# Optimization experiments

Measured on AMD Instinct MI355X. Metric: run time of the kernel, lower is better.

## Reference

```python
import jax, jax.numpy as jnp
import numpy as np

BLOCK = 128  # block_size=(128,128) from MoeFP8Matmul
E, H, I = 8, 2048, 2816  # experts, hidden, intermediate
T, K = 512, 2  # tokens, top-k

_FP8 = getattr(jnp, "float8_e4m3fn", jnp.float32)

def _dequant(w, s):
    # w: [N, Kd] fp8 values (stored fp32), s: [N//128, Kd//128] inverse scales
    s_full = jnp.repeat(jnp.repeat(s, BLOCK, axis=-2), BLOCK, axis=-1)
    return w * s_full

def setup_inputs() -> dict:
    key = jax.random.key(0)
    ks = jax.random.split(key, 7)
    x = jax.random.normal(ks[0], (T, H), dtype=jnp.float32)
    topk_ids = jax.random.randint(ks[1], (T, K), 0, E, dtype=jnp.int64)
    topk_weights = jax.random.uniform(ks[2], (T, K), dtype=jnp.float32)
    # fp8-representable weight values (round-trip through e4m3)
    w13 = (jax.random.normal(ks[3], (E, 2 * I, H), dtype=jnp.float32) * 0.5)
    w13_fp8 = w13.astype(_FP8).astype(jnp.float32)
    w2 = (jax.random.normal(ks[4], (E, H, I), dtype=jnp.float32) * 0.5)
    w2_fp8 = w2.astype(_FP8).astype(jnp.float32)
    w13_scale = jax.random.uniform(ks[5], (E, (2 * I) // BLOCK, H // BLOCK),
                                   dtype=jnp.float32, minval=0.5, maxval=1.5)
    w2_scale = jax.random.uniform(ks[6], (E, H // BLOCK, I // BLOCK),
                                  dtype=jnp.float32, minval=0.5, maxval=1.5)
    return {"x": x, "topk_ids": topk_ids, "topk_weights": topk_weights,
            "w13_fp8": w13_fp8, "w13_scale": w13_scale,
            "w2_fp8": w2_fp8, "w2_scale": w2_scale}

def reference(x, topk_ids, topk_weights, w13_fp8, w13_scale, w2_fp8, w2_scale):
    # Per-expert block-FP8 dequant then grouped SwiGLU MoE GEMM, weighted-summed by router.
    out = jnp.zeros_like(x)
    for e in range(E):  # small fixed expert count
        W13 = _dequant(w13_fp8[e], w13_scale[e])   # [2I, H]
        W2 = _dequant(w2_fp8[e], w2_scale[e])      # [H, I]
        h = x @ W13.T                              # [T, 2I]
        gate, up = jnp.split(h, 2, axis=-1)
        act = jax.nn.silu(gate) * up               # [T, I]
        oe = act @ W2.T                            # [T, H]
        coef = jnp.sum(jnp.where(topk_ids == e, topk_weights, 0.0), axis=-1)  # [T]
        out = out + coef[:, None] * oe
    return out
```

## Files before the change

kernel.cpp:

```cpp
#include <hip/hip_runtime.h>
#include <hip/hip_bf16.h>
#include <cstdint>
#include <cstddef>

#define E_   8
#define H_   2048
#define I_   2816
#define T_   512
#define NPAIR 1024

#define TM   192
#define TN   32
#define BK   64
#define LDSB 72
#define MT_  3

typedef __attribute__((ext_vector_type(8))) short          bf16x8;
typedef __attribute__((ext_vector_type(4))) float          f32x4;
typedef __attribute__((ext_vector_type(8))) unsigned short u16x8;

__device__ __forceinline__ unsigned short f2bf(float f){
  union { float f; unsigned u; } a; a.f = f;
  unsigned u = a.u;
  unsigned r = u + 0x7fffu + ((u >> 16) & 1u);
  return (unsigned short)(r >> 16);
}

__device__ __forceinline__ void cvt4(u16x8& dst, int base, const float4 v, float s){
  __hip_bfloat162 p0 = __float22bfloat162_rn(float2{v.x*s, v.y*s});
  __hip_bfloat162 p1 = __float22bfloat162_rn(float2{v.z*s, v.w*s});
  union { __hip_bfloat162 b; unsigned u; } a0{p0}, a1{p1};
  dst[base+0] = (unsigned short)(a0.u & 0xffff);
  dst[base+1] = (unsigned short)(a0.u >> 16);
  dst[base+2] = (unsigned short)(a1.u & 0xffff);
  dst[base+3] = (unsigned short)(a1.u >> 16);
}

__device__ __forceinline__ void sync_lds(){
  asm volatile("s_waitcnt lgkmcnt(0)\n\ts_barrier" ::: "memory");
}

__global__ void route_kernel(const int* __restrict__ ids,
                             int* __restrict__ offs, int* __restrict__ ptok,
                             int* __restrict__ sop){
  __shared__ int scnt[E_];
  __shared__ int scur[E_];
  const int tid = threadIdx.x;
  if (tid < E_) scnt[tid] = 0;
  __syncthreads();
  const int e = ids[tid];
  atomicAdd(&scnt[e], 1);
  __syncthreads();
  if (tid == 0){
    int s = 0;
    for (int i = 0; i < E_; i++){ offs[i] = s; scur[i] = s; s += scnt[i]; }
    offs[E_] = s;
  }
  __syncthreads();
  const int pos = atomicAdd(&scur[e], 1);
  ptok[pos] = tid >> 1;
  sop[tid]  = pos;
}

__global__ void prep_kernel(const float* __restrict__ x, const int* __restrict__ ptok,
                            unsigned short* __restrict__ xg){
  const int slot = blockIdx.x;
  const int tok  = ptok[slot];
  const int k0   = threadIdx.x * 8;
  const float4 v0 = *(const float4*)(x + (size_t)tok*H_ + k0);
  const float4 v1 = *(const float4*)(x + (size_t)tok*H_ + k0 + 4);
  u16x8 o;
  cvt4(o, 0, v0, 1.f);
  cvt4(o, 4, v1, 1.f);
  *(u16x8*)(xg + (size_t)slot*H_ + k0) = o;
}

__global__ __launch_bounds__(256, 3)
void gemm1_kernel(const unsigned short* __restrict__ xg, const float* __restrict__ w13,
                  const float* __restrict__ s13, const int* __restrict__ offs,
                  unsigned short* __restrict__ act)
{
  const int e   = blockIdx.x;
  const int off = offs[e];
  const int cnt = offs[e+1] - off;
  const int m0  = blockIdx.z * TM;
  if (m0 >= cnt) return;
  const int rows = min(TM, cnt - m0);
  const int nb   = blockIdx.y * TN;

  __shared__ __align__(16) unsigned short Bs[2][2*TN][LDSB];

  const int tid  = threadIdx.x;
  const int wave = tid >> 6;
  const int lane = tid & 63;
  const int quad = lane >> 4;
  const int l16  = lane & 15;

  const float* w13e = w13 + (size_t)e * (2*I_) * H_;
  const float* s13e = s13 + (size_t)e * (2*I_/128) * (H_/128);

  const int br = tid >> 2;
  const int bc = tid & 3;
  const int grow = (br < TN) ? (nb + br) : (I_ + nb + (br - TN));
  const float* bp = w13e + (size_t)grow * H_ + bc*16;
  const int srow  = (((br < TN) ? 0 : (I_/128)) + (nb >> 7)) * (H_/128);

  const unsigned short* aP[MT_];
  #pragma unroll
  for (int mt = 0; mt < MT_; mt++){
    int sl = off + m0 + wave*(TM/4) + mt*16 + l16;
    sl = min(sl, NPAIR - 1);
    aP[mt] = xg + (size_t)sl * H_ + quad*8;
  }

  f32x4 acc[2][MT_][2];
  #pragma unroll
  for (int h = 0; h < 2; h++)
    #pragma unroll
    for (int mt = 0; mt < MT_; mt++)
      #pragma unroll
      for (int nt = 0; nt < 2; nt++)
        acc[h][mt][nt] = (f32x4){0.f, 0.f, 0.f, 0.f};

  float4 R0[4], R1[4];
  bf16x8 A0[2][MT_], A1[2][MT_];
  float  sE, sO;

  auto loadB = [&](int t, float4* R){
    const float* p = bp + t*BK;
    #pragma unroll
    for (int j = 0; j < 4; j++) R[j] = *(const float4*)(p + j*4);
  };
  auto loadA = [&](int t, bf16x8 (*A)[MT_]){
    #pragma unroll
    for (int kk = 0; kk < 2; kk++)
      #pragma unroll
      for (int mt = 0; mt < MT_; mt++)
        A[kk][mt] = *(const bf16x8*)(aP[mt] + t*BK + kk*32);
  };
  auto storeB = [&](const float4* R, float s, int buf){
    u16x8 w0, w1;
    cvt4(w0, 0, R[0], s); cvt4(w0, 4, R[1], s);
    cvt4(w1, 0, R[2], s); cvt4(w1, 4, R[3], s);
    *(u16x8*)&Bs[buf][br][bc*16]     = w0;
    *(u16x8*)&Bs[buf][br][bc*16 + 8] = w1;
  };
  auto mfma = [&](int buf, bf16x8 (*A)[MT_]){
    #pragma unroll
    for (int kk = 0; kk < 2; kk++)
      #pragma unroll
      for (int hh = 0; hh < 2; hh++)
        #pragma unroll
        for (int nt = 0; nt < 2; nt++){
          bf16x8 bv = *(const bf16x8*)&Bs[buf][hh*TN + nt*16 + l16][kk*32 + quad*8];
          #pragma unroll
          for (int mt = 0; mt < MT_; mt++)
            acc[hh][mt][nt] = __builtin_amdgcn_mfma_f32_16x16x32_bf16(A[kk][mt], bv, acc[hh][mt][nt], 0, 0, 0);
        }
  };

  const int NITER = H_/BK;
  loadB(0, R0); sE = s13e[srow];
  loadB(1, R1); sO = s13e[srow];
  loadA(0, A0);
  storeB(R0, sE, 0);
  sync_lds();

  for (int i = 0; i < NITER; i += 2){
    if (i+2 < NITER){ loadB(i+2, R0); sE = s13e[srow + ((i+2) >> 1)]; }
    loadA(i+1, A1);
    mfma(0, A0);
    storeB(R1, sO, 1);
    sync_lds();
    if (i+3 < NITER){ loadB(i+3, R1); sO = s13e[srow + ((i+3) >> 1)]; }
    if (i+2 < NITER) loadA(i+2, A0);
    mfma(1, A1);
    if (i+2 < NITER){ storeB(R0, sE, 0); sync_lds(); }
  }

  #pragma unroll
  for (int mt = 0; mt < MT_; mt++){
    #pragma unroll
    for (int nt = 0; nt < 2; nt++){
      #pragma unroll
      for (int r = 0; r < 4; r++){
        const int m = wave*(TM/4) + mt*16 + quad*4 + r;
        if (m < rows){
          const float g = acc[0][mt][nt][r];
          const float u = acc[1][mt][nt][r];
          const float sg = g / (1.f + __expf(-g));
          act[(size_t)(off + m0 + m)*I_ + (nb + nt*16 + l16)] = f2bf(sg * u);
        }
      }
    }
  }
}

__global__ __launch_bounds__(256, 3)
void gemm2_kernel(const unsigned short* __restrict__ act, const float* __restrict__ w2,
                  const float* __restrict__ s2, const int* __restrict__ offs,
                  float* __restrict__ buf)
{
  const int e   = blockIdx.x;
  const int off = offs[e];
  const int cnt = offs[e+1] - off;
  const int m0  = blockIdx.z * TM;
  if (m0 >= cnt) return;
  const int rows = min(TM, cnt - m0);
  const int nb   = blockIdx.y * TN;

  __shared__ __align__(16) unsigned short Bs[2][TN][LDSB];

  const int tid  = threadIdx.x;
  const int wave = tid >> 6;
  const int lane = tid & 63;
  const int quad = lane >> 4;
  const int l16  = lane & 15;

  const float* w2e = w2 + (size_t)e * H_ * I_;
  const float* s2e = s2 + (size_t)e * (H_/128) * (I_/128);

  const int br = tid >> 3;
  const int bc = tid & 7;
  const float* bp = w2e + (size_t)(nb + br) * I_ + bc*8;
  const int srow  = (nb >> 7) * (I_/128);

  const unsigned short* aP[MT_];
  #pragma unroll
  for (int mt = 0; mt < MT_; mt++){
    int sl = off + m0 + wave*(TM/4) + mt*16 + l16;
    sl = min(sl, NPAIR - 1);
    aP[mt] = act + (size_t)sl * I_ + quad*8;
  }

  f32x4 acc[MT_][2];
  #pragma unroll
  for (int mt = 0; mt < MT_; mt++)
    #pragma unroll
    for (int nt = 0; nt < 2; nt++)
      acc[mt][nt] = (f32x4){0.f, 0.f, 0.f, 0.f};

  float4 R0[2], R1[2];
  bf16x8 A0[2][MT_], A1[2][MT_];
  float  sE, sO;

  auto loadB = [&](int t, float4* R){
    const float* p = bp + t*BK;
    #pragma unroll
    for (int j = 0; j < 2; j++) R[j] = *(const float4*)(p + j*4);
  };
  auto loadA = [&](int t, bf16x8 (*A)[MT_]){
    #pragma unroll
    for (int kk = 0; kk < 2; kk++)
      #pragma unroll
      for (int mt = 0; mt < MT_; mt++)
        A[kk][mt] = *(const bf16x8*)(aP[mt] + t*BK + kk*32);
  };
  auto storeB = [&](const float4* R, float s, int buf_i){
    u16x8 w0;
    cvt4(w0, 0, R[0], s); cvt4(w0, 4, R[1], s);
    *(u16x8*)&Bs[buf_i][br][bc*8] = w0;
  };
  auto mfma = [&](int buf_i, bf16x8 (*A)[MT_]){
    #pragma unroll
    for (int kk = 0; kk < 2; kk++)
      #pragma unroll
      for (int nt = 0; nt < 2; nt++){
        bf16x8 bv = *(const bf16x8*)&Bs[buf_i][nt*16 + l16][kk*32 + quad*8];
        #pragma unroll
        for (int mt = 0; mt < MT_; mt++)
          acc[mt][nt] = __builtin_amdgcn_mfma_f32_16x16x32_bf16(A[kk][mt], bv, acc[mt][nt], 0, 0, 0);
      }
  };

  const int NITER = I_/BK;
  loadB(0, R0); sE = s2e[srow];
  loadB(1, R1); sO = s2e[srow];
  loadA(0, A0);
  storeB(R0, sE, 0);
  sync_lds();

  for (int i = 0; i < NITER; i += 2){
    if (i+2 < NITER){ loadB(i+2, R0); sE = s2e[srow + ((i+2) >> 1)]; }
    loadA(i+1, A1);
    mfma(0, A0);
    storeB(R1, sO, 1);
    sync_lds();
    if (i+3 < NITER){ loadB(i+3, R1); sO = s2e[srow + ((i+3) >> 1)]; }
    if (i+2 < NITER) loadA(i+2, A0);
    mfma(1, A1);
    if (i+2 < NITER){ storeB(R0, sE, 0); sync_lds(); }
  }

  #pragma unroll
  for (int mt = 0; mt < MT_; mt++){
    #pragma unroll
    for (int nt = 0; nt < 2; nt++){
      #pragma unroll
      for (int r = 0; r < 4; r++){
        const int m = wave*(TM/4) + mt*16 + quad*4 + r;
        if (m < rows)
          buf[(size_t)(off + m0 + m)*H_ + (nb + nt*16 + l16)] = acc[mt][nt][r];
      }
    }
  }
}

__global__ void combine_kernel(const float* __restrict__ buf, const int* __restrict__ sop,
                               const float* __restrict__ tw, float* __restrict__ out){
  const int gid = blockIdx.x*256 + threadIdx.x;
  const int t = gid >> 9;
  const int c = gid & 511;
  const int s0 = sop[2*t], s1 = sop[2*t+1];
  const float w0 = tw[2*t], w1 = tw[2*t+1];
  const float4 v0 = ((const float4*)buf)[(size_t)s0*(H_/4) + c];
  const float4 v1 = ((const float4*)buf)[(size_t)s1*(H_/4) + c];
  float4 o;
  o.x = w0*v0.x + w1*v1.x;
  o.y = w0*v0.y + w1*v1.y;
  o.z = w0*v0.z + w1*v1.z;
  o.w = w0*v0.w + w1*v1.w;
  ((float4*)out)[gid] = o;
}

extern "C" void kernel_launch(void* const* d_in, const int* in_sizes, int n_in,
                              void* d_out, int out_size, void* d_ws, size_t ws_size,
                              hipStream_t stream){
  const float* x   = (const float*)d_in[0];
  const int*   ids = (const int*)  d_in[1];
  const float* tw  = (const float*)d_in[2];
  const float* w13 = (const float*)d_in[3];
  const float* s13 = (const float*)d_in[4];
  const float* w2  = (const float*)d_in[5];
  const float* s2  = (const float*)d_in[6];
  float* out = (float*)d_out;

  char* ws = (char*)d_ws;
  int* offs = (int*)ws;
  int* ptok = (int*)(ws + 64);
  int* sop  = (int*)(ws + 64 + 4096);
  unsigned short* xg  = (unsigned short*)(ws + 16384);
  float*          buf = (float*)(ws + 16384);
  unsigned short* act = (unsigned short*)(ws + 16384 + (size_t)NPAIR*H_*4);

  route_kernel  <<<1, NPAIR, 0, stream>>>(ids, offs, ptok, sop);
  prep_kernel   <<<NPAIR, 256, 0, stream>>>(x, ptok, xg);
  gemm1_kernel  <<<dim3(E_, I_/TN, (NPAIR + TM - 1)/TM), 256, 0, stream>>>(xg, w13, s13, offs, act);
  gemm2_kernel  <<<dim3(E_, H_/TN, (NPAIR + TM - 1)/TM), 256, 0, stream>>>(act, w2, s2, offs, buf);
  combine_kernel<<<(T_*H_/4)/256, 256, 0, stream>>>(buf, sop, tw, out);
}
```

Measured before the change: 692.4 us.

## Load B weights directly into registers, dropping LDS staging and barriers

Both GEMM kernels stop staging dequantized fp32 weight tiles through LDS. Each lane now loads its own 8-wide weight fragment from global memory, scales it, converts it to bf16 in registers, and feeds it straight to MFMA, so the LDS writes, reads and barriers go away. The N tile is halved to 16 so every wave loads the same B fragment, and the grid doubles along N. The cost is that the four waves of a block each fetch identical B data from global memory (relying on cache), lanes do narrower, less coalesced 32-byte row reads, and more blocks reload the A operand.

```diff
diff --git a/kernel.cpp b/kernel.cpp
--- a/kernel.cpp
+++ b/kernel.cpp
@@ -10,9 +10,8 @@
 #define NPAIR 1024
 
 #define TM   192
-#define TN   32
+#define TN   16
 #define BK   64
-#define LDSB 72
 #define MT_  3
 
 typedef __attribute__((ext_vector_type(8))) short          bf16x8;
@@ -36,8 +35,8 @@
   dst[base+3] = (unsigned short)(a1.u >> 16);
 }
 
-__device__ __forceinline__ void sync_lds(){
-  asm volatile("s_waitcnt lgkmcnt(0)\n\ts_barrier" ::: "memory");
+__device__ __forceinline__ bf16x8 u2b(u16x8 v){
+  union { u16x8 u; bf16x8 b; } x; x.u = v; return x.b;
 }
 
 __global__ void route_kernel(const int* __restrict__ ids,
@@ -88,8 +87,6 @@
   const int rows = min(TM, cnt - m0);
   const int nb   = blockIdx.y * TN;
 
-  __shared__ __align__(16) unsigned short Bs[2][2*TN][LDSB];
-
   const int tid  = threadIdx.x;
   const int wave = tid >> 6;
   const int lane = tid & 63;
@@ -99,11 +96,11 @@
   const float* w13e = w13 + (size_t)e * (2*I_) * H_;
   const float* s13e = s13 + (size_t)e * (2*I_/128) * (H_/128);
 
-  const int br = tid >> 2;
-  const int bc = tid & 3;
-  const int grow = (br < TN) ? (nb + br) : (I_ + nb + (br - TN));
-  const float* bp = w13e + (size_t)grow * H_ + bc*16;
-  const int srow  = (((br < TN) ? 0 : (I_/128)) + (nb >> 7)) * (H_/128);
+  const float* bP[2];
+  bP[0] = w13e + (size_t)(nb + l16) * H_ + quad*8;
+  bP[1] = w13e + (size_t)(I_ + nb + l16) * H_ + quad*8;
+  const int s0row = (nb >> 7) * (H_/128);
+  const int s1row = ((I_/128) + (nb >> 7)) * (H_/128);
 
   const unsigned short* aP[MT_];
   #pragma unroll
@@ -113,23 +110,23 @@
     aP[mt] = xg + (size_t)sl * H_ + quad*8;
   }
 
-  f32x4 acc[2][MT_][2];
+  f32x4 acc[2][MT_];
   #pragma unroll
   for (int h = 0; h < 2; h++)
     #pragma unroll
     for (int mt = 0; mt < MT_; mt++)
-      #pragma unroll
-      for (int nt = 0; nt < 2; nt++)
-        acc[h][mt][nt] = (f32x4){0.f, 0.f, 0.f, 0.f};
-
-  float4 R0[4], R1[4];
+      acc[h][mt] = (f32x4){0.f, 0.f, 0.f, 0.f};
+
+  float4 S0[4], S1[4];
   bf16x8 A0[2][MT_], A1[2][MT_];
-  float  sE, sO;
-
-  auto loadB = [&](int t, float4* R){
-    const float* p = bp + t*BK;
-    #pragma unroll
-    for (int j = 0; j < 4; j++) R[j] = *(const float4*)(p + j*4);
+
+  auto loadBhalf = [&](int t, int kk, float4* S){
+    #pragma unroll
+    for (int hh = 0; hh < 2; hh++){
+      const float* p = bP[hh] + t*BK + kk*32;
+      S[2*hh]   = *(const float4*)p;
+      S[2*hh+1] = *(const float4*)(p + 4);
+    }
   };
   auto loadA = [&](int t, bf16x8 (*A)[MT_]){
     #pragma unroll
@@ -138,59 +135,50 @@
       for (int mt = 0; mt < MT_; mt++)
         A[kk][mt] = *(const bf16x8*)(aP[mt] + t*BK + kk*32);
   };
-  auto storeB = [&](const float4* R, float s, int buf){
-    u16x8 w0, w1;
-    cvt4(w0, 0, R[0], s); cvt4(w0, 4, R[1], s);
-    cvt4(w1, 0, R[2], s); cvt4(w1, 4, R[3], s);
-    *(u16x8*)&Bs[buf][br][bc*16]     = w0;
-    *(u16x8*)&Bs[buf][br][bc*16 + 8] = w1;
-  };
-  auto mfma = [&](int buf, bf16x8 (*A)[MT_]){
-    #pragma unroll
-    for (int kk = 0; kk < 2; kk++)
+  auto mfmaHalf = [&](int kk, bf16x8 (*A)[MT_], const float4* S, float sg, float su){
+    #pragma unroll
+    for (int hh = 0; hh < 2; hh++){
+      u16x8 o;
+      const float s = hh ? su : sg;
+      cvt4(o, 0, S[2*hh],   s);
+      cvt4(o, 4, S[2*hh+1], s);
+      const bf16x8 bv = u2b(o);
       #pragma unroll
-      for (int hh = 0; hh < 2; hh++)
-        #pragma unroll
-        for (int nt = 0; nt < 2; nt++){
-          bf16x8 bv = *(const bf16x8*)&Bs[buf][hh*TN + nt*16 + l16][kk*32 + quad*8];
-          #pragma unroll
-          for (int mt = 0; mt < MT_; mt++)
-            acc[hh][mt][nt] = __builtin_amdgcn_mfma_f32_16x16x32_bf16(A[kk][mt], bv, acc[hh][mt][nt], 0, 0, 0);
-        }
+      for (int mt = 0; mt < MT_; mt++)
+        acc[hh][mt] = __builtin_amdgcn_mfma_f32_16x16x32_bf16(A[kk][mt], bv, acc[hh][mt], 0, 0, 0);
+    }
   };
 
   const int NITER = H_/BK;
-  loadB(0, R0); sE = s13e[srow];
-  loadB(1, R1); sO = s13e[srow];
+  loadBhalf(0, 0, S0);
+  loadBhalf(0, 1, S1);
   loadA(0, A0);
-  storeB(R0, sE, 0);
-  sync_lds();
-
-  for (int i = 0; i < NITER; i += 2){
-    if (i+2 < NITER){ loadB(i+2, R0); sE = s13e[srow + ((i+2) >> 1)]; }
-    loadA(i+1, A1);
-    mfma(0, A0);
-    storeB(R1, sO, 1);
-    sync_lds();
-    if (i+3 < NITER){ loadB(i+3, R1); sO = s13e[srow + ((i+3) >> 1)]; }
-    if (i+2 < NITER) loadA(i+2, A0);
-    mfma(1, A1);
-    if (i+2 < NITER){ storeB(R0, sE, 0); sync_lds(); }
+
+  for (int t = 0; t < NITER; t += 2){
+    const float sg = s13e[s0row + (t >> 1)];
+    const float su = s13e[s1row + (t >> 1)];
+    loadA(t+1, A1);
+    mfmaHalf(0, A0, S0, sg, su);
+    loadBhalf(t+1, 0, S0);
+    mfmaHalf(1, A0, S1, sg, su);
+    loadBhalf(t+1, 1, S1);
+    if (t+2 < NITER) loadA(t+2, A0);
+    mfmaHalf(0, A1, S0, sg, su);
+    if (t+2 < NITER) loadBhalf(t+2, 0, S0);
+    mfmaHalf(1, A1, S1, sg, su);
+    if (t+2 < NITER) loadBhalf(t+2, 1, S1);
   }
 
   #pragma unroll
   for (int mt = 0; mt < MT_; mt++){
     #pragma unroll
-    for (int nt = 0; nt < 2; nt++){
-      #pragma unroll
-      for (int r = 0; r < 4; r++){
-        const int m = wave*(TM/4) + mt*16 + quad*4 + r;
-        if (m < rows){
-          const float g = acc[0][mt][nt][r];
-          const float u = acc[1][mt][nt][r];
-          const float sg = g / (1.f + __expf(-g));
-          act[(size_t)(off + m0 + m)*I_ + (nb + nt*16 + l16)] = f2bf(sg * u);
-        }
+    for (int r = 0; r < 4; r++){
+      const int m = wave*(TM/4) + mt*16 + quad*4 + r;
+      if (m < rows){
+        const float g = acc[0][mt][r];
+        const float u = acc[1][mt][r];
+        const float sg2 = g / (1.f + __expf(-g));
+        act[(size_t)(off + m0 + m)*I_ + (nb + l16)] = f2bf(sg2 * u);
       }
     }
   }
@@ -209,8 +197,6 @@
   const int rows = min(TM, cnt - m0);
   const int nb   = blockIdx.y * TN;
 
-  __shared__ __align__(16) unsigned short Bs[2][TN][LDSB];
-
   const int tid  = threadIdx.x;
   const int wave = tid >> 6;
   const int lane = tid & 63;
@@ -220,9 +206,7 @@
   const float* w2e = w2 + (size_t)e * H_ * I_;
   const float* s2e = s2 + (size_t)e * (H_/128) * (I_/128);
 
-  const int br = tid >> 3;
-  const int bc = tid & 7;
-  const float* bp = w2e + (size_t)(nb + br) * I_ + bc*8;
+  const float* bP = w2e + (size_t)(nb + l16) * I_ + quad*8;
   const int srow  = (nb >> 7) * (I_/128);
 
   const unsigned short* aP[MT_];
@@ -233,21 +217,18 @@
     aP[mt] = act + (size_t)sl * I_ + quad*8;
   }
 
-  f32x4 acc[MT_][2];
+  f32x4 acc[MT_];
   #pragma unroll
   for (int mt = 0; mt < MT_; mt++)
-    #pragma unroll
-    for (int nt = 0; nt < 2; nt++)
-      acc[mt][nt] = (f32x4){0.f, 0.f, 0.f, 0.f};
-
-  float4 R0[2], R1[2];
+    acc[mt] = (f32x4){0.f, 0.f, 0.f, 0.f};
+
+  float4 S0[2], S1[2];
   bf16x8 A0[2][MT_], A1[2][MT_];
-  float  sE, sO;
-
-  auto loadB = [&](int t, float4* R){
-    const float* p = bp + t*BK;
-    #pragma unroll
-    for (int j = 0; j < 2; j++) R[j] = *(const float4*)(p + j*4);
+
+  auto loadBhalf = [&](int t, int kk, float4* S){
+    const float* p = bP + t*BK + kk*32;
+    S[0] = *(const float4*)p;
+    S[1] = *(const float4*)(p + 4);
   };
   auto loadA = [&](int t, bf16x8 (*A)[MT_]){
     #pragma unroll
@@ -256,52 +237,42 @@
       for (int mt = 0; mt < MT_; mt++)
         A[kk][mt] = *(const bf16x8*)(aP[mt] + t*BK + kk*32);
   };
-  auto storeB = [&](const float4* R, float s, int buf_i){
-    u16x8 w0;
-    cvt4(w0, 0, R[0], s); cvt4(w0, 4, R[1], s);
-    *(u16x8*)&Bs[buf_i][br][bc*8] = w0;
-  };
-  auto mfma = [&](int buf_i, bf16x8 (*A)[MT_]){
-    #pragma unroll
-    for (int kk = 0; kk < 2; kk++)
-      #pragma unroll
-      for (int nt = 0; nt < 2; nt++){
-        bf16x8 bv = *(const bf16x8*)&Bs[buf_i][nt*16 + l16][kk*32 + quad*8];
-        #pragma unroll
-        for (int mt = 0; mt < MT_; mt++)
-          acc[mt][nt] = __builtin_amdgcn_mfma_f32_16x16x32_bf16(A[kk][mt], bv, acc[mt][nt], 0, 0, 0);
-      }
+  auto mfmaHalf = [&](int kk, bf16x8 (*A)[MT_], const float4* S, float s){
+    u16x8 o;
+    cvt4(o, 0, S[0], s);
+    cvt4(o, 4, S[1], s);
+    const bf16x8 bv = u2b(o);
+    #pragma unroll
+    for (int mt = 0; mt < MT_; mt++)
+      acc[mt] = __builtin_amdgcn_mfma_f32_16x16x32_bf16(A[kk][mt], bv, acc[mt], 0, 0, 0);
   };
 
   const int NITER = I_/BK;
-  loadB(0, R0); sE = s2e[srow];
-  loadB(1, R1); sO = s2e[srow];
+  loadBhalf(0, 0, S0);
+  loadBhalf(0, 1, S1);
   loadA(0, A0);
-  storeB(R0, sE, 0);
-  sync_lds();
-
-  for (int i = 0; i < NITER; i += 2){
-    if (i+2 < NITER){ loadB(i+2, R0); sE = s2e[srow + ((i+2) >> 1)]; }
-    loadA(i+1, A1);
-    mfma(0, A0);
-    storeB(R1, sO, 1);
-    sync_lds();
-    if (i+3 < NITER){ loadB(i+3, R1); sO = s2e[srow + ((i+3) >> 1)]; }
-    if (i+2 < NITER) loadA(i+2, A0);
-    mfma(1, A1);
-    if (i+2 < NITER){ storeB(R0, sE, 0); sync_lds(); }
+
+  for (int t = 0; t < NITER; t += 2){
+    const float s = s2e[srow + (t >> 1)];
+    loadA(t+1, A1);
+    mfmaHalf(0, A0, S0, s);
+    loadBhalf(t+1, 0, S0);
+    mfmaHalf(1, A0, S1, s);
+    loadBhalf(t+1, 1, S1);
+    if (t+2 < NITER) loadA(t+2, A0);
+    mfmaHalf(0, A1, S0, s);
+    if (t+2 < NITER) loadBhalf(t+2, 0, S0);
+    mfmaHalf(1, A1, S1, s);
+    if (t+2 < NITER) loadBhalf(t+2, 1, S1);
   }
 
   #pragma unroll
   for (int mt = 0; mt < MT_; mt++){
     #pragma unroll
-    for (int nt = 0; nt < 2; nt++){
-      #pragma unroll
-      for (int r = 0; r < 4; r++){
-        const int m = wave*(TM/4) + mt*16 + quad*4 + r;
-        if (m < rows)
-          buf[(size_t)(off + m0 + m)*H_ + (nb + nt*16 + l16)] = acc[mt][nt][r];
-      }
+    for (int r = 0; r < 4; r++){
+      const int m = wave*(TM/4) + mt*16 + quad*4 + r;
+      if (m < rows)
+        buf[(size_t)(off + m0 + m)*H_ + (nb + l16)] = acc[mt][r];
     }
   }
 }
```

New measurement: 946.2 us. +36.7%, slower.

## Stream fp32 weights directly into LDS with triple-buffered async loads

Applied to the files above, without the earlier changes.

Both GEMM kernels now fetch the fp32 weight tiles with global_load_lds, writing straight into a three-slot LDS ring with an XOR swizzle, instead of loading into registers, converting to bf16 and storing. The scale multiply and bf16 conversion move to the consumer side, applied after reading from LDS right before each MFMA. Synchronisation becomes vmcnt waits plus one barrier per k-step. This removes register staging and the VGPR-to-LDS store from the load path, at the cost of twice the LDS footprint (fp32), more LDS read traffic, and redundant per-wave conversion work.

```diff
diff --git a/kernel.cpp b/kernel.cpp
--- a/kernel.cpp
+++ b/kernel.cpp
@@ -12,7 +12,6 @@
 #define TM   192
 #define TN   32
 #define BK   64
-#define LDSB 72
 #define MT_  3
 
 typedef __attribute__((ext_vector_type(8))) short          bf16x8;
@@ -36,8 +35,14 @@
   dst[base+3] = (unsigned short)(a1.u >> 16);
 }
 
-__device__ __forceinline__ void sync_lds(){
-  asm volatile("s_waitcnt lgkmcnt(0)\n\ts_barrier" ::: "memory");
+__device__ __forceinline__ bf16x8 u2b(u16x8 v){
+  union { u16x8 u; bf16x8 b; } x; x.u = v; return x.b;
+}
+
+__device__ __forceinline__ void gload_lds16(const void* g, void* l){
+  __builtin_amdgcn_global_load_lds(
+      (const __attribute__((address_space(1))) unsigned int*)g,
+      (__attribute__((address_space(3))) unsigned int*)l, 16, 0, 0);
 }
 
 __global__ void route_kernel(const int* __restrict__ ids,
@@ -88,10 +93,10 @@
   const int rows = min(TM, cnt - m0);
   const int nb   = blockIdx.y * TN;
 
-  __shared__ __align__(16) unsigned short Bs[2][2*TN][LDSB];
+  __shared__ __align__(16) float Bs[3][2*TN][BK];
 
   const int tid  = threadIdx.x;
-  const int wave = tid >> 6;
+  const int wv   = tid >> 6;
   const int lane = tid & 63;
   const int quad = lane >> 4;
   const int l16  = lane & 15;
@@ -99,16 +104,27 @@
   const float* w13e = w13 + (size_t)e * (2*I_) * H_;
   const float* s13e = s13 + (size_t)e * (2*I_/128) * (H_/128);
 
-  const int br = tid >> 2;
-  const int bc = tid & 3;
-  const int grow = (br < TN) ? (nb + br) : (I_ + nb + (br - TN));
-  const float* bp = w13e + (size_t)grow * H_ + bc*16;
-  const int srow  = (((br < TN) ? 0 : (I_/128)) + (nb >> 7)) * (H_/128);
+  const int s0row = (nb >> 7) * (H_/128);
+  const int s1row = ((I_/128) + (nb >> 7)) * (H_/128);
+
+  const char* srcP[4];
+  #pragma unroll
+  for (int j = 0; j < 4; j++){
+    const int rl = wv*16 + j*4 + (lane >> 4);
+    const int gr = (rl < TN) ? (nb + rl) : (I_ + nb + (rl - TN));
+    const int cb = ((lane & 15) << 4) ^ ((rl & 7) << 4);
+    srcP[j] = (const char*)(w13e + (size_t)gr * H_) + cb;
+  }
+  auto stage = [&](int t, int slot){
+    #pragma unroll
+    for (int j = 0; j < 4; j++)
+      gload_lds16(srcP[j] + (size_t)t * (BK*4), &Bs[slot][wv*16 + j*4][0]);
+  };
 
   const unsigned short* aP[MT_];
   #pragma unroll
   for (int mt = 0; mt < MT_; mt++){
-    int sl = off + m0 + wave*(TM/4) + mt*16 + l16;
+    int sl = off + m0 + wv*(TM/4) + mt*16 + l16;
     sl = min(sl, NPAIR - 1);
     aP[mt] = xg + (size_t)sl * H_ + quad*8;
   }
@@ -122,15 +138,7 @@
       for (int nt = 0; nt < 2; nt++)
         acc[h][mt][nt] = (f32x4){0.f, 0.f, 0.f, 0.f};
 
-  float4 R0[4], R1[4];
   bf16x8 A0[2][MT_], A1[2][MT_];
-  float  sE, sO;
-
-  auto loadB = [&](int t, float4* R){
-    const float* p = bp + t*BK;
-    #pragma unroll
-    for (int j = 0; j < 4; j++) R[j] = *(const float4*)(p + j*4);
-  };
   auto loadA = [&](int t, bf16x8 (*A)[MT_]){
     #pragma unroll
     for (int kk = 0; kk < 2; kk++)
@@ -138,44 +146,56 @@
       for (int mt = 0; mt < MT_; mt++)
         A[kk][mt] = *(const bf16x8*)(aP[mt] + t*BK + kk*32);
   };
-  auto storeB = [&](const float4* R, float s, int buf){
-    u16x8 w0, w1;
-    cvt4(w0, 0, R[0], s); cvt4(w0, 4, R[1], s);
-    cvt4(w1, 0, R[2], s); cvt4(w1, 4, R[3], s);
-    *(u16x8*)&Bs[buf][br][bc*16]     = w0;
-    *(u16x8*)&Bs[buf][br][bc*16 + 8] = w1;
-  };
-  auto mfma = [&](int buf, bf16x8 (*A)[MT_]){
+
+  auto comp = [&](int slot, bf16x8 (*A)[MT_], float sg, float su){
     #pragma unroll
     for (int kk = 0; kk < 2; kk++)
       #pragma unroll
-      for (int hh = 0; hh < 2; hh++)
+      for (int hh = 0; hh < 2; hh++){
+        const float s = hh ? su : sg;
         #pragma unroll
         for (int nt = 0; nt < 2; nt++){
-          bf16x8 bv = *(const bf16x8*)&Bs[buf][hh*TN + nt*16 + l16][kk*32 + quad*8];
+          const int row = hh*TN + nt*16 + l16;
+          const int xr  = (row & 7) << 2;
+          const int cb  = kk*32 + quad*8;
+          const float4 F0 = *(const float4*)&Bs[slot][row][cb ^ xr];
+          const float4 F1 = *(const float4*)&Bs[slot][row][(cb + 4) ^ xr];
+          u16x8 o; cvt4(o, 0, F0, s); cvt4(o, 4, F1, s);
+          const bf16x8 bv = u2b(o);
           #pragma unroll
           for (int mt = 0; mt < MT_; mt++)
             acc[hh][mt][nt] = __builtin_amdgcn_mfma_f32_16x16x32_bf16(A[kk][mt], bv, acc[hh][mt][nt], 0, 0, 0);
         }
+      }
   };
 
   const int NITER = H_/BK;
-  loadB(0, R0); sE = s13e[srow];
-  loadB(1, R1); sO = s13e[srow];
   loadA(0, A0);
-  storeB(R0, sE, 0);
-  sync_lds();
-
-  for (int i = 0; i < NITER; i += 2){
-    if (i+2 < NITER){ loadB(i+2, R0); sE = s13e[srow + ((i+2) >> 1)]; }
-    loadA(i+1, A1);
-    mfma(0, A0);
-    storeB(R1, sO, 1);
-    sync_lds();
-    if (i+3 < NITER){ loadB(i+3, R1); sO = s13e[srow + ((i+3) >> 1)]; }
-    if (i+2 < NITER) loadA(i+2, A0);
-    mfma(1, A1);
-    if (i+2 < NITER){ storeB(R0, sE, 0); sync_lds(); }
+  stage(0, 0);
+  stage(1, 1);
+  asm volatile("s_waitcnt vmcnt(4)" ::: "memory");
+  __builtin_amdgcn_s_barrier();
+  stage(2, 2);
+  loadA(1, A1);
+  comp(0, A0, s13e[s0row], s13e[s1row]);
+
+  int cs = 1, ss = 0;
+  for (int t = 1; t < NITER-1; t++){
+    asm volatile("s_waitcnt vmcnt(10)" ::: "memory");
+    __builtin_amdgcn_s_barrier();
+    if (t+2 < NITER) stage(t+2, ss);
+    loadA(t+1, (t & 1) ? A0 : A1);
+    const float sg = s13e[s0row + (t >> 1)];
+    const float su = s13e[s1row + (t >> 1)];
+    comp(cs, (t & 1) ? A1 : A0, sg, su);
+    cs = (cs == 2) ? 0 : cs + 1;
+    ss = (ss == 2) ? 0 : ss + 1;
+  }
+  {
+    asm volatile("s_waitcnt vmcnt(6)" ::: "memory");
+    __builtin_amdgcn_s_barrier();
+    const int t = NITER-1;
+    comp(cs, (t & 1) ? A1 : A0, s13e[s0row + (t >> 1)], s13e[s1row + (t >> 1)]);
   }
 
   #pragma unroll
@@ -184,12 +204,12 @@
     for (int nt = 0; nt < 2; nt++){
       #pragma unroll
       for (int r = 0; r < 4; r++){
-        const int m = wave*(TM/4) + mt*16 + quad*4 + r;
+        const int m = wv*(TM/4) + mt*16 + quad*4 + r;
         if (m < rows){
           const float g = acc[0][mt][nt][r];
           const float u = acc[1][mt][nt][r];
-          const float sg = g / (1.f + __expf(-g));
-          act[(size_t)(off + m0 + m)*I_ + (nb + nt*16 + l16)] = f2bf(sg * u);
+          const float sg2 = g / (1.f + __expf(-g));
+          act[(size_t)(off + m0 + m)*I_ + (nb + nt*16 + l16)] = f2bf(sg2 * u);
         }
       }
     }
@@ -209,26 +229,35 @@
   const int rows = min(TM, cnt - m0);
   const int nb   = blockIdx.y * TN;
 
-  __shared__ __align__(16) unsigned short Bs[2][TN][LDSB];
+  __shared__ __align__(16) float Bs[3][TN][BK];
 
   const int tid  = threadIdx.x;
-  const int wave = tid >> 6;
+  const int wv   = tid >> 6;
   const int lane = tid & 63;
   const int quad = lane >> 4;
   const int l16  = lane & 15;
 
   const float* w2e = w2 + (size_t)e * H_ * I_;
   const float* s2e = s2 + (size_t)e * (H_/128) * (I_/128);
-
-  const int br = tid >> 3;
-  const int bc = tid & 7;
-  const float* bp = w2e + (size_t)(nb + br) * I_ + bc*8;
   const int srow  = (nb >> 7) * (I_/128);
 
+  const char* srcP[2];
+  #pragma unroll
+  for (int j = 0; j < 2; j++){
+    const int rl = wv*8 + j*4 + (lane >> 4);
+    const int cb = ((lane & 15) << 4) ^ ((rl & 7) << 4);
+    srcP[j] = (const char*)(w2e + (size_t)(nb + rl) * I_) + cb;
+  }
+  auto stage = [&](int t, int slot){
+    #pragma unroll
+    for (int j = 0; j < 2; j++)
+      gload_lds16(srcP[j] + (size_t)t * (BK*4), &Bs[slot][wv*8 + j*4][0]);
+  };
+
   const unsigned short* aP[MT_];
   #pragma unroll
   for (int mt = 0; mt < MT_; mt++){
-    int sl = off + m0 + wave*(TM/4) + mt*16 + l16;
+    int sl = off + m0 + wv*(TM/4) + mt*16 + l16;
     sl = min(sl, NPAIR - 1);
     aP[mt] = act + (size_t)sl * I_ + quad*8;
   }
@@ -240,15 +269,7 @@
     for (int nt = 0; nt < 2; nt++)
       acc[mt][nt] = (f32x4){0.f, 0.f, 0.f, 0.f};
 
-  float4 R0[2], R1[2];
   bf16x8 A0[2][MT_], A1[2][MT_];
-  float  sE, sO;
-
-  auto loadB = [&](int t, float4* R){
-    const float* p = bp + t*BK;
-    #pragma unroll
-    for (int j = 0; j < 2; j++) R[j] = *(const float4*)(p + j*4);
-  };
   auto loadA = [&](int t, bf16x8 (*A)[MT_]){
     #pragma unroll
     for (int kk = 0; kk < 2; kk++)
@@ -256,17 +277,19 @@
       for (int mt = 0; mt < MT_; mt++)
         A[kk][mt] = *(const bf16x8*)(aP[mt] + t*BK + kk*32);
   };
-  auto storeB = [&](const float4* R, float s, int buf_i){
-    u16x8 w0;
-    cvt4(w0, 0, R[0], s); cvt4(w0, 4, R[1], s);
-    *(u16x8*)&Bs[buf_i][br][bc*8] = w0;
-  };
-  auto mfma = [&](int buf_i, bf16x8 (*A)[MT_]){
+
+  auto comp = [&](int slot, bf16x8 (*A)[MT_], float s){
     #pragma unroll
     for (int kk = 0; kk < 2; kk++)
       #pragma unroll
       for (int nt = 0; nt < 2; nt++){
-        bf16x8 bv = *(const bf16x8*)&Bs[buf_i][nt*16 + l16][kk*32 + quad*8];
+        const int row = nt*16 + l16;
+        const int xr  = (row & 7) << 2;
+        const int cb  = kk*32 + quad*8;
+        const float4 F0 = *(const float4*)&Bs[slot][row][cb ^ xr];
+        const float4 F1 = *(const float4*)&Bs[slot][row][(cb + 4) ^ xr];
+        u16x8 o; cvt4(o, 0, F0, s); cvt4(o, 4, F1, s);
+        const bf16x8 bv = u2b(o);
         #pragma unroll
         for (int mt = 0; mt < MT_; mt++)
           acc[mt][nt] = __builtin_amdgcn_mfma_f32_16x16x32_bf16(A[kk][mt], bv, acc[mt][nt], 0, 0, 0);
@@ -274,22 +297,30 @@
   };
 
   const int NITER = I_/BK;
-  loadB(0, R0); sE = s2e[srow];
-  loadB(1, R1); sO = s2e[srow];
   loadA(0, A0);
-  storeB(R0, sE, 0);
-  sync_lds();
-
-  for (int i = 0; i < NITER; i += 2){
-    if (i+2 < NITER){ loadB(i+2, R0); sE = s2e[srow + ((i+2) >> 1)]; }
-    loadA(i+1, A1);
-    mfma(0, A0);
-    storeB(R1, sO, 1);
-    sync_lds();
-    if (i+3 < NITER){ loadB(i+3, R1); sO = s2e[srow + ((i+3) >> 1)]; }
-    if (i+2 < NITER) loadA(i+2, A0);
-    mfma(1, A1);
-    if (i+2 < NITER){ storeB(R0, sE, 0); sync_lds(); }
+  stage(0, 0);
+  stage(1, 1);
+  asm volatile("s_waitcnt vmcnt(2)" ::: "memory");
+  __builtin_amdgcn_s_barrier();
+  stage(2, 2);
+  loadA(1, A1);
+  comp(0, A0, s2e[srow]);
+
+  int cs = 1, ss = 0;
+  for (int t = 1; t < NITER-1; t++){
+    asm volatile("s_waitcnt vmcnt(8)" ::: "memory");
+    __builtin_amdgcn_s_barrier();
+    if (t+2 < NITER) stage(t+2, ss);
+    loadA(t+1, (t & 1) ? A0 : A1);
+    comp(cs, (t & 1) ? A1 : A0, s2e[srow + (t >> 1)]);
+    cs = (cs == 2) ? 0 : cs + 1;
+    ss = (ss == 2) ? 0 : ss + 1;
+  }
+  {
+    asm volatile("s_waitcnt vmcnt(6)" ::: "memory");
+    __builtin_amdgcn_s_barrier();
+    const int t = NITER-1;
+    comp(cs, (t & 1) ? A1 : A0, s2e[srow + (t >> 1)]);
   }
 
   #pragma unroll
@@ -298,7 +329,7 @@
     for (int nt = 0; nt < 2; nt++){
       #pragma unroll
       for (int r = 0; r < 4; r++){
-        const int m = wave*(TM/4) + mt*16 + quad*4 + r;
+        const int m = wv*(TM/4) + mt*16 + quad*4 + r;
         if (m < rows)
           buf[(size_t)(off + m0 + m)*H_ + (nb + nt*16 + l16)] = acc[mt][nt][r];
       }
```

New measurement: 700.9 us. About the same (+1.2%).

## Fuse prep, both GEMMs and combine into one persistent kernel with grid barriers

Applied to the files above, without the earlier changes.

Replaces the four separate prep, gemm1, gemm2 and combine launches with a single persistent 768-block kernel that moves between stages through software grid barriers built on atomics. The prep stage now converts each token once and gemm1 gathers rows through ptok. Gemm2 is re-tiled to 64x16 tiles, and each block loops over N-tiles and M-halves so it covers every expert's rows. This removes launch gaps and the tail of each stage, but depends on all 768 blocks being resident at once and adds spin-barrier overhead.

```diff
diff --git a/kernel.cpp b/kernel.cpp
--- a/kernel.cpp
+++ b/kernel.cpp
@@ -3,17 +3,20 @@
 #include <cstdint>
 #include <cstddef>
 
-#define E_   8
-#define H_   2048
-#define I_   2816
-#define T_   512
+#define E_    8
+#define H_    2048
+#define I_    2816
+#define T_    512
 #define NPAIR 1024
-
-#define TM   192
-#define TN   32
+#define GRID_ 768
+
+#define TM1  192
+#define TN1  32
+#define MT1  3
+#define TM2  64
+#define TN2  16
 #define BK   64
 #define LDSB 72
-#define MT_  3
 
 typedef __attribute__((ext_vector_type(8))) short          bf16x8;
 typedef __attribute__((ext_vector_type(4))) float          f32x4;
@@ -40,13 +43,26 @@
   asm volatile("s_waitcnt lgkmcnt(0)\n\ts_barrier" ::: "memory");
 }
 
+__device__ __forceinline__ void gridbar(int* bar){
+  __syncthreads();
+  if (threadIdx.x == 0){
+    __threadfence();
+    __hip_atomic_fetch_add(bar, 1, __ATOMIC_ACQ_REL, __HIP_MEMORY_SCOPE_AGENT);
+    while (__hip_atomic_load(bar, __ATOMIC_ACQUIRE, __HIP_MEMORY_SCOPE_AGENT) < GRID_)
+      __builtin_amdgcn_s_sleep(2);
+  }
+  __syncthreads();
+  __threadfence();
+}
+
 __global__ void route_kernel(const int* __restrict__ ids,
                              int* __restrict__ offs, int* __restrict__ ptok,
-                             int* __restrict__ sop){
+                             int* __restrict__ sop, int* __restrict__ bar){
   __shared__ int scnt[E_];
   __shared__ int scur[E_];
   const int tid = threadIdx.x;
   if (tid < E_) scnt[tid] = 0;
+  if (tid < 4)  bar[tid] = 0;
   __syncthreads();
   const int e = ids[tid];
   atomicAdd(&scnt[e], 1);
@@ -62,265 +78,243 @@
   sop[tid]  = pos;
 }
 
-__global__ void prep_kernel(const float* __restrict__ x, const int* __restrict__ ptok,
-                            unsigned short* __restrict__ xg){
-  const int slot = blockIdx.x;
-  const int tok  = ptok[slot];
-  const int k0   = threadIdx.x * 8;
-  const float4 v0 = *(const float4*)(x + (size_t)tok*H_ + k0);
-  const float4 v1 = *(const float4*)(x + (size_t)tok*H_ + k0 + 4);
-  u16x8 o;
-  cvt4(o, 0, v0, 1.f);
-  cvt4(o, 4, v1, 1.f);
-  *(u16x8*)(xg + (size_t)slot*H_ + k0) = o;
-}
-
 __global__ __launch_bounds__(256, 3)
-void gemm1_kernel(const unsigned short* __restrict__ xg, const float* __restrict__ w13,
-                  const float* __restrict__ s13, const int* __restrict__ offs,
-                  unsigned short* __restrict__ act)
+void moe_kernel(const float* __restrict__ x,
+                const float* __restrict__ w13, const float* __restrict__ s13,
+                const float* __restrict__ w2,  const float* __restrict__ s2,
+                const float* __restrict__ tw,
+                const int* __restrict__ offs, const int* __restrict__ ptok,
+                const int* __restrict__ sop,  int* __restrict__ bar,
+                unsigned short* __restrict__ xg, unsigned short* __restrict__ act,
+                float* __restrict__ buf, float* __restrict__ out)
 {
-  const int e   = blockIdx.x;
-  const int off = offs[e];
-  const int cnt = offs[e+1] - off;
-  const int m0  = blockIdx.z * TM;
-  if (m0 >= cnt) return;
-  const int rows = min(TM, cnt - m0);
-  const int nb   = blockIdx.y * TN;
-
-  __shared__ __align__(16) unsigned short Bs[2][2*TN][LDSB];
-
+  const int b    = blockIdx.x;
   const int tid  = threadIdx.x;
-  const int wave = tid >> 6;
+  const int wv   = tid >> 6;
   const int lane = tid & 63;
   const int quad = lane >> 4;
   const int l16  = lane & 15;
 
-  const float* w13e = w13 + (size_t)e * (2*I_) * H_;
-  const float* s13e = s13 + (size_t)e * (2*I_/128) * (H_/128);
-
-  const int br = tid >> 2;
-  const int bc = tid & 3;
-  const int grow = (br < TN) ? (nb + br) : (I_ + nb + (br - TN));
-  const float* bp = w13e + (size_t)grow * H_ + bc*16;
-  const int srow  = (((br < TN) ? 0 : (I_/128)) + (nb >> 7)) * (H_/128);
-
-  const unsigned short* aP[MT_];
-  #pragma unroll
-  for (int mt = 0; mt < MT_; mt++){
-    int sl = off + m0 + wave*(TM/4) + mt*16 + l16;
-    sl = min(sl, NPAIR - 1);
-    aP[mt] = xg + (size_t)sl * H_ + quad*8;
-  }
-
-  f32x4 acc[2][MT_][2];
-  #pragma unroll
-  for (int h = 0; h < 2; h++)
-    #pragma unroll
-    for (int mt = 0; mt < MT_; mt++)
-      #pragma unroll
-      for (int nt = 0; nt < 2; nt++)
-        acc[h][mt][nt] = (f32x4){0.f, 0.f, 0.f, 0.f};
-
-  float4 R0[4], R1[4];
-  bf16x8 A0[2][MT_], A1[2][MT_];
-  float  sE, sO;
-
-  auto loadB = [&](int t, float4* R){
-    const float* p = bp + t*BK;
-    #pragma unroll
-    for (int j = 0; j < 4; j++) R[j] = *(const float4*)(p + j*4);
-  };
-  auto loadA = [&](int t, bf16x8 (*A)[MT_]){
-    #pragma unroll
-    for (int kk = 0; kk < 2; kk++)
-      #pragma unroll
-      for (int mt = 0; mt < MT_; mt++)
-        A[kk][mt] = *(const bf16x8*)(aP[mt] + t*BK + kk*32);
-  };
-  auto storeB = [&](const float4* R, float s, int buf){
-    u16x8 w0, w1;
-    cvt4(w0, 0, R[0], s); cvt4(w0, 4, R[1], s);
-    cvt4(w1, 0, R[2], s); cvt4(w1, 4, R[3], s);
-    *(u16x8*)&Bs[buf][br][bc*16]     = w0;
-    *(u16x8*)&Bs[buf][br][bc*16 + 8] = w1;
-  };
-  auto mfma = [&](int buf, bf16x8 (*A)[MT_]){
-    #pragma unroll
-    for (int kk = 0; kk < 2; kk++)
-      #pragma unroll
-      for (int hh = 0; hh < 2; hh++)
+  __shared__ __align__(16) unsigned short Bs[2][2*TN1][LDSB];
+
+  if (b < T_){
+    const int k0 = tid * 8;
+    const float4 v0 = *(const float4*)(x + (size_t)b*H_ + k0);
+    const float4 v1 = *(const float4*)(x + (size_t)b*H_ + k0 + 4);
+    u16x8 o;
+    cvt4(o, 0, v0, 1.f);
+    cvt4(o, 4, v1, 1.f);
+    *(u16x8*)(xg + (size_t)b*H_ + k0) = o;
+  }
+  gridbar(bar + 0);
+
+  {
+    const int e = b & 7;
+    const int q = b >> 3;
+    if (q < I_/TN1){
+      const int nb  = q * TN1;
+      const int off = offs[e];
+      const int cnt = offs[e+1] - off;
+
+      const float* w13e = w13 + (size_t)e * (2*I_) * H_;
+      const float* s13e = s13 + (size_t)e * 44 * 16;
+
+      const int br = tid >> 2;
+      const int bc = tid & 3;
+      const int grow = (br < TN1) ? (nb + br) : (I_ + nb + (br - TN1));
+      const float* bp = w13e + (size_t)grow * H_ + bc*16;
+      const int srow  = (((br < TN1) ? 0 : 22) + (nb >> 7)) * 16;
+
+      for (int m0 = 0; m0 < cnt; m0 += TM1){
+        const int rows = min(TM1, cnt - m0);
+
+        const unsigned short* aP[MT1];
         #pragma unroll
-        for (int nt = 0; nt < 2; nt++){
-          bf16x8 bv = *(const bf16x8*)&Bs[buf][hh*TN + nt*16 + l16][kk*32 + quad*8];
-          #pragma unroll
-          for (int mt = 0; mt < MT_; mt++)
-            acc[hh][mt][nt] = __builtin_amdgcn_mfma_f32_16x16x32_bf16(A[kk][mt], bv, acc[hh][mt][nt], 0, 0, 0);
-        }
-  };
-
-  const int NITER = H_/BK;
-  loadB(0, R0); sE = s13e[srow];
-  loadB(1, R1); sO = s13e[srow];
-  loadA(0, A0);
-  storeB(R0, sE, 0);
-  sync_lds();
-
-  for (int i = 0; i < NITER; i += 2){
-    if (i+2 < NITER){ loadB(i+2, R0); sE = s13e[srow + ((i+2) >> 1)]; }
-    loadA(i+1, A1);
-    mfma(0, A0);
-    storeB(R1, sO, 1);
-    sync_lds();
-    if (i+3 < NITER){ loadB(i+3, R1); sO = s13e[srow + ((i+3) >> 1)]; }
-    if (i+2 < NITER) loadA(i+2, A0);
-    mfma(1, A1);
-    if (i+2 < NITER){ storeB(R0, sE, 0); sync_lds(); }
-  }
-
-  #pragma unroll
-  for (int mt = 0; mt < MT_; mt++){
-    #pragma unroll
-    for (int nt = 0; nt < 2; nt++){
-      #pragma unroll
-      for (int r = 0; r < 4; r++){
-        const int m = wave*(TM/4) + mt*16 + quad*4 + r;
-        if (m < rows){
-          const float g = acc[0][mt][nt][r];
-          const float u = acc[1][mt][nt][r];
-          const float sg = g / (1.f + __expf(-g));
-          act[(size_t)(off + m0 + m)*I_ + (nb + nt*16 + l16)] = f2bf(sg * u);
+        for (int mt = 0; mt < MT1; mt++){
+          int sl = off + m0 + wv*(TM1/4) + mt*16 + l16;
+          sl = min(sl, NPAIR - 1);
+          aP[mt] = xg + (size_t)ptok[sl] * H_ + quad*8;
+        }
+
+        f32x4 acc[2][MT1][2];
+        #pragma unroll
+        for (int h = 0; h < 2; h++)
+          #pragma unroll
+          for (int mt = 0; mt < MT1; mt++)
+            #pragma unroll
+            for (int nt = 0; nt < 2; nt++)
+              acc[h][mt][nt] = (f32x4){0.f, 0.f, 0.f, 0.f};
+
+        float4 R0[4], R1[4];
+        bf16x8 A0[2][MT1], A1[2][MT1];
+        float  sE, sO;
+
+        auto loadB = [&](int t, float4* R){
+          const float* p = bp + t*BK;
+          #pragma unroll
+          for (int j = 0; j < 4; j++) R[j] = *(const float4*)(p + j*4);
+        };
+        auto loadA = [&](int t, bf16x8 (*A)[MT1]){
+          #pragma unroll
+          for (int kk = 0; kk < 2; kk++)
+            #pragma unroll
+            for (int mt = 0; mt < MT1; mt++)
+              A[kk][mt] = *(const bf16x8*)(aP[mt] + t*BK + kk*32);
+        };
+        auto storeB = [&](const float4* R, float s, int bi){
+          u16x8 w0, w1;
+          cvt4(w0, 0, R[0], s); cvt4(w0, 4, R[1], s);
+          cvt4(w1, 0, R[2], s); cvt4(w1, 4, R[3], s);
+          *(u16x8*)&Bs[bi][br][bc*16]     = w0;
+          *(u16x8*)&Bs[bi][br][bc*16 + 8] = w1;
+        };
+        auto mfma = [&](int bi, bf16x8 (*A)[MT1]){
+          #pragma unroll
+          for (int kk = 0; kk < 2; kk++)
+            #pragma unroll
+            for (int hh = 0; hh < 2; hh++)
+              #pragma unroll
+              for (int nt = 0; nt < 2; nt++){
+                bf16x8 bv = *(const bf16x8*)&Bs[bi][hh*TN1 + nt*16 + l16][kk*32 + quad*8];
+                #pragma unroll
+                for (int mt = 0; mt < MT1; mt++)
+                  acc[hh][mt][nt] = __builtin_amdgcn_mfma_f32_16x16x32_bf16(A[kk][mt], bv, acc[hh][mt][nt], 0, 0, 0);
+              }
+        };
+
+        const int NITER = H_/BK;
+        loadB(0, R0); sE = s13e[srow];
+        loadB(1, R1); sO = s13e[srow];
+        loadA(0, A0);
+        storeB(R0, sE, 0);
+        sync_lds();
+        for (int i = 0; i < NITER; i += 2){
+          if (i+2 < NITER){ loadB(i+2, R0); sE = s13e[srow + ((i+2) >> 1)]; }
+          loadA(i+1, A1);
+          mfma(0, A0);
+          storeB(R1, sO, 1);
+          sync_lds();
+          if (i+3 < NITER){ loadB(i+3, R1); sO = s13e[srow + ((i+3) >> 1)]; }
+          if (i+2 < NITER) loadA(i+2, A0);
+          mfma(1, A1);
+          if (i+2 < NITER){ storeB(R0, sE, 0); sync_lds(); }
+        }
+
+        #pragma unroll
+        for (int mt = 0; mt < MT1; mt++){
+          #pragma unroll
+          for (int nt = 0; nt < 2; nt++){
+            #pragma unroll
+            for (int r = 0; r < 4; r++){
+              const int m = wv*(TM1/4) + mt*16 + quad*4 + r;
+              if (m < rows){
+                const float g = acc[0][mt][nt][r];
+                const float u = acc[1][mt][nt][r];
+                const float sg = g / (1.f + __expf(-g));
+                act[(size_t)(off + m0 + m)*I_ + (nb + nt*16 + l16)] = f2bf(sg * u);
+              }
+            }
+          }
         }
       }
     }
   }
-}
-
-__global__ __launch_bounds__(256, 3)
-void gemm2_kernel(const unsigned short* __restrict__ act, const float* __restrict__ w2,
-                  const float* __restrict__ s2, const int* __restrict__ offs,
-                  float* __restrict__ buf)
-{
-  const int e   = blockIdx.x;
-  const int off = offs[e];
-  const int cnt = offs[e+1] - off;
-  const int m0  = blockIdx.z * TM;
-  if (m0 >= cnt) return;
-  const int rows = min(TM, cnt - m0);
-  const int nb   = blockIdx.y * TN;
-
-  __shared__ __align__(16) unsigned short Bs[2][TN][LDSB];
-
-  const int tid  = threadIdx.x;
-  const int wave = tid >> 6;
-  const int lane = tid & 63;
-  const int quad = lane >> 4;
-  const int l16  = lane & 15;
-
-  const float* w2e = w2 + (size_t)e * H_ * I_;
-  const float* s2e = s2 + (size_t)e * (H_/128) * (I_/128);
-
-  const int br = tid >> 3;
-  const int bc = tid & 7;
-  const float* bp = w2e + (size_t)(nb + br) * I_ + bc*8;
-  const int srow  = (nb >> 7) * (I_/128);
-
-  const unsigned short* aP[MT_];
-  #pragma unroll
-  for (int mt = 0; mt < MT_; mt++){
-    int sl = off + m0 + wave*(TM/4) + mt*16 + l16;
-    sl = min(sl, NPAIR - 1);
-    aP[mt] = act + (size_t)sl * I_ + quad*8;
-  }
-
-  f32x4 acc[MT_][2];
-  #pragma unroll
-  for (int mt = 0; mt < MT_; mt++)
-    #pragma unroll
-    for (int nt = 0; nt < 2; nt++)
-      acc[mt][nt] = (f32x4){0.f, 0.f, 0.f, 0.f};
-
-  float4 R0[2], R1[2];
-  bf16x8 A0[2][MT_], A1[2][MT_];
-  float  sE, sO;
-
-  auto loadB = [&](int t, float4* R){
-    const float* p = bp + t*BK;
-    #pragma unroll
-    for (int j = 0; j < 2; j++) R[j] = *(const float4*)(p + j*4);
-  };
-  auto loadA = [&](int t, bf16x8 (*A)[MT_]){
-    #pragma unroll
-    for (int kk = 0; kk < 2; kk++)
-      #pragma unroll
-      for (int mt = 0; mt < MT_; mt++)
-        A[kk][mt] = *(const bf16x8*)(aP[mt] + t*BK + kk*32);
-  };
-  auto storeB = [&](const float4* R, float s, int buf_i){
-    u16x8 w0;
-    cvt4(w0, 0, R[0], s); cvt4(w0, 4, R[1], s);
-    *(u16x8*)&Bs[buf_i][br][bc*8] = w0;
-  };
-  auto mfma = [&](int buf_i, bf16x8 (*A)[MT_]){
-    #pragma unroll
-    for (int kk = 0; kk < 2; kk++)
-      #pragma unroll
-      for (int nt = 0; nt < 2; nt++){
-        bf16x8 bv = *(const bf16x8*)&Bs[buf_i][nt*16 + l16][kk*32 + quad*8];
+  gridbar(bar + 1);
+
+  {
+    const int e   = b & 7;
+    const int off = offs[e];
+    const int cnt = offs[e+1] - off;
+    const float* w2e = w2 + (size_t)e * H_ * I_;
+    const float* s2e = s2 + (size_t)e * 16 * 22;
+    auto Bs2 = reinterpret_cast<unsigned short (*)[TN2][LDSB]>(&Bs[0][0][0]);
+
+    const int br2 = tid >> 4;
+    const int bc2 = tid & 15;
+
+    for (int r = (b >> 3); r < 256; r += 96){
+      const int nb = (r & 127) * TN2;
+      const int mh = r >> 7;
+      const float* bp = w2e + (size_t)(nb + br2) * I_ + bc2*4;
+      const int srow  = (nb >> 7) * 22;
+
+      for (int m0 = mh*TM2; m0 < cnt; m0 += 2*TM2){
+        const int rows = min(TM2, cnt - m0);
+
+        int sl = off + m0 + wv*16 + l16;
+        sl = min(sl, NPAIR - 1);
+        const unsigned short* aP = act + (size_t)sl * I_ + quad*8;
+
+        f32x4 acc2 = (f32x4){0.f, 0.f, 0.f, 0.f};
+
+        float4 R0, R1;
+        bf16x8 A0[2], A1[2];
+        float  sE, sO;
+
+        auto loadB = [&](int t, float4& R){ R = *(const float4*)(bp + t*BK); };
+        auto loadA = [&](int t, bf16x8* A){
+          #pragma unroll
+          for (int kk = 0; kk < 2; kk++)
+            A[kk] = *(const bf16x8*)(aP + t*BK + kk*32);
+        };
+        auto storeB = [&](float4 R, float s, int bi){
+          u16x8 w; cvt4(w, 0, R, s);
+          uint2 v;
+          v.x = (unsigned)w[0] | ((unsigned)w[1] << 16);
+          v.y = (unsigned)w[2] | ((unsigned)w[3] << 16);
+          *(uint2*)&Bs2[bi][br2][bc2*4] = v;
+        };
+        auto mfma = [&](int bi, bf16x8* A){
+          #pragma unroll
+          for (int kk = 0; kk < 2; kk++){
+            bf16x8 bv = *(const bf16x8*)&Bs2[bi][l16][kk*32 + quad*8];
+            acc2 = __builtin_amdgcn_mfma_f32_16x16x32_bf16(A[kk], bv, acc2, 0, 0, 0);
+          }
+        };
+
+        const int NITER = I_/BK;
+        loadB(0, R0); sE = s2e[srow];
+        loadB(1, R1); sO = s2e[srow];
+        loadA(0, A0);
+        storeB(R0, sE, 0);
+        sync_lds();
+        for (int i = 0; i < NITER; i += 2){
+          if (i+2 < NITER){ loadB(i+2, R0); sE = s2e[srow + ((i+2) >> 1)]; }
+          loadA(i+1, A1);
+          mfma(0, A0);
+          storeB(R1, sO, 1);
+          sync_lds();
+          if (i+3 < NITER){ loadB(i+3, R1); sO = s2e[srow + ((i+3) >> 1)]; }
+          if (i+2 < NITER) loadA(i+2, A0);
+          mfma(1, A1);
+          if (i+2 < NITER){ storeB(R0, sE, 0); sync_lds(); }
+        }
+
         #pragma unroll
-        for (int mt = 0; mt < MT_; mt++)
-          acc[mt][nt] = __builtin_amdgcn_mfma_f32_16x16x32_bf16(A[kk][mt], bv, acc[mt][nt], 0, 0, 0);
-      }
-  };
-
-  const int NITER = I_/BK;
-  loadB(0, R0); sE = s2e[srow];
-  loadB(1, R1); sO = s2e[srow];
-  loadA(0, A0);
-  storeB(R0, sE, 0);
-  sync_lds();
-
-  for (int i = 0; i < NITER; i += 2){
-    if (i+2 < NITER){ loadB(i+2, R0); sE = s2e[srow + ((i+2) >> 1)]; }
-    loadA(i+1, A1);
-    mfma(0, A0);
-    storeB(R1, sO, 1);
-    sync_lds();
-    if (i+3 < NITER){ loadB(i+3, R1); sO = s2e[srow + ((i+3) >> 1)]; }
-    if (i+2 < NITER) loadA(i+2, A0);
-    mfma(1, A1);
-    if (i+2 < NITER){ storeB(R0, sE, 0); sync_lds(); }
-  }
-
-  #pragma unroll
-  for (int mt = 0; mt < MT_; mt++){
-    #pragma unroll
-    for (int nt = 0; nt < 2; nt++){
-      #pragma unroll
-      for (int r = 0; r < 4; r++){
-        const int m = wave*(TM/4) + mt*16 + quad*4 + r;
-        if (m < rows)
-          buf[(size_t)(off + m0 + m)*H_ + (nb + nt*16 + l16)] = acc[mt][nt][r];
+        for (int rr = 0; rr < 4; rr++){
+          const int m = wv*16 + quad*4 + rr;
+          if (m < rows)
+            buf[(size_t)(off + m0 + m)*H_ + (nb + l16)] = acc2[rr];
+        }
       }
     }
   }
-}
-
-__global__ void combine_kernel(const float* __restrict__ buf, const int* __restrict__ sop,
-                               const float* __restrict__ tw, float* __restrict__ out){
-  const int gid = blockIdx.x*256 + threadIdx.x;
-  const int t = gid >> 9;
-  const int c = gid & 511;
-  const int s0 = sop[2*t], s1 = sop[2*t+1];
-  const float w0 = tw[2*t], w1 = tw[2*t+1];
-  const float4 v0 = ((const float4*)buf)[(size_t)s0*(H_/4) + c];
-  const float4 v1 = ((const float4*)buf)[(size_t)s1*(H_/4) + c];
-  float4 o;
-  o.x = w0*v0.x + w1*v1.x;
-  o.y = w0*v0.y + w1*v1.y;
-  o.z = w0*v0.z + w1*v1.z;
-  o.w = w0*v0.w + w1*v1.w;
-  ((float4*)out)[gid] = o;
+  gridbar(bar + 2);
+
+  for (int i = b*256 + tid; i < T_*(H_/4); i += GRID_*256){
+    const int t = i >> 9;
+    const int c = i & 511;
+    const int s0 = sop[2*t], s1 = sop[2*t+1];
+    const float w0 = tw[2*t], w1 = tw[2*t+1];
+    const float4 v0 = ((const float4*)buf)[(size_t)s0*(H_/4) + c];
+    const float4 v1 = ((const float4*)buf)[(size_t)s1*(H_/4) + c];
+    float4 o;
+    o.x = w0*v0.x + w1*v1.x;
+    o.y = w0*v0.y + w1*v1.y;
+    o.z = w0*v0.z + w1*v1.z;
+    o.w = w0*v0.w + w1*v1.w;
+    ((float4*)out)[i] = o;
+  }
 }
 
 extern "C" void kernel_launch(void* const* d_in, const int* in_sizes, int n_in,
@@ -337,15 +331,15 @@
 
   char* ws = (char*)d_ws;
   int* offs = (int*)ws;
-  int* ptok = (int*)(ws + 64);
-  int* sop  = (int*)(ws + 64 + 4096);
+  int* bar  = (int*)(ws + 128);
+  int* ptok = (int*)(ws + 256);
+  int* sop  = (int*)(ws + 256 + 4096);
   unsigned short* xg  = (unsigned short*)(ws + 16384);
-  float*          buf = (float*)(ws + 16384);
-  unsigned short* act = (unsigned short*)(ws + 16384 + (size_t)NPAIR*H_*4);
-
-  route_kernel  <<<1, NPAIR, 0, stream>>>(ids, offs, ptok, sop);
-  prep_kernel   <<<NPAIR, 256, 0, stream>>>(x, ptok, xg);
-  gemm1_kernel  <<<dim3(E_, I_/TN, (NPAIR + TM - 1)/TM), 256, 0, stream>>>(xg, w13, s13, offs, act);
-  gemm2_kernel  <<<dim3(E_, H_/TN, (NPAIR + TM - 1)/TM), 256, 0, stream>>>(act, w2, s2, offs, buf);
-  combine_kernel<<<(T_*H_/4)/256, 256, 0, stream>>>(buf, sop, tw, out);
-}
+  unsigned short* act = (unsigned short*)(ws + 16384 + 2097152);
+  float*          buf = (float*)(ws + 16384 + 2097152 + 5767168);
+
+  route_kernel<<<1, NPAIR, 0, stream>>>(ids, offs, ptok, sop, bar);
+  moe_kernel  <<<GRID_, 256, 0, stream>>>(x, w13, s13, w2, s2, tw,
+                                          offs, ptok, sop, bar,
+                                          xg, act, buf, out);
+}
```

After: 1.589 ms. 129% more time.
